# Kernel tuning notes

Measured on AMD Instinct MI355X. Metric: run time of the kernel, lower is better.

Reference implementation:

```python
import jax, jax.numpy as jnp
import numpy as np

K = 7          # local attention kernel size
PAD = 3        # (K-1)//2 so output spatial dims match input
GROUPS = 8

def unfold2d(x, k):
    # x: [B, C, H+k-1, W+k-1] -> patches [B, C, H, W, k*k] (kh-major, kw-minor, matching F.unfold)
    B, C, Hp, Wp = x.shape
    H, W = Hp - k + 1, Wp - k + 1
    return jnp.stack([x[:, :, i:i + H, j:j + W] for i in range(k) for j in range(k)], axis=-1)

def setup_inputs():
    key = jax.random.key(0)
    k1, k2, k3, k4, k5, k6 = jax.random.split(key, 6)
    B, Cin, H, W = 2, 256, 56, 56
    outc = 256
    scale = (2.0 / Cin) ** 0.5  # kaiming fan_out-ish init
    return {
        "feature_map": jax.random.normal(k1, (B, 2 * Cin, H, W), jnp.float32),
        "w_q": jax.random.normal(k2, (outc, Cin), jnp.float32) * scale,
        "w_k": jax.random.normal(k3, (outc, Cin), jnp.float32) * scale,
        "w_v": jax.random.normal(k4, (outc, Cin), jnp.float32) * scale,
        "rel_h": jax.random.normal(k5, (outc // 2, K), jnp.float32),
        "rel_w": jax.random.normal(k6, (outc // 2, K), jnp.float32),
    }

def reference(feature_map, w_q, w_k, w_v, rel_h, rel_w):
    B, C2, H, W = feature_map.shape
    Cin = C2 // 2
    fm_t0, fm_t1 = feature_map[:, :Cin], feature_map[:, Cin:]
    outc = w_q.shape[0]
    # 1x1 convs (bias=False)
    q = jnp.einsum('oc,bchw->bohw', w_q, fm_t1)                      # [B, outc, H, W]
    padded = jnp.pad(fm_t0, ((0, 0), (0, 0), (PAD, PAD), (PAD, PAD)))
    kk = jnp.einsum('oc,bchw->bohw', w_k, padded)
    vv = jnp.einsum('oc,bchw->bohw', w_v, padded)
    k_out = unfold2d(kk, K)                                          # [B, outc, H, W, K*K]
    v_out = unfold2d(vv, K)
    # relative position bias: first half channels get row bias, second half col bias
    half = outc // 2
    bias_h = jnp.broadcast_to(rel_h[:, :, None], (half, K, K)).reshape(half, K * K)
    bias_w = jnp.broadcast_to(rel_w[:, None, :], (half, K, K)).reshape(half, K * K)
    bias = jnp.concatenate([bias_h, bias_w], axis=0)                 # [outc, K*K]
    k_out = k_out + bias[None, :, None, None, :]
    G, Cg = GROUPS, outc // GROUPS
    qg = q.reshape(B, G, Cg, H, W)
    kg = k_out.reshape(B, G, Cg, H, W, K * K)
    vg = v_out.reshape(B, G, Cg, H, W, K * K)
    logits = jnp.einsum('bgchw,bgchwk->bghwk', qg, kg)
    wts = jax.nn.softmax(logits, axis=-1)
    out = jnp.einsum('bghwk,bgchwk->bgchw', wts, vg)
    return out.reshape(B, outc, H, W)
```

## Files before the change

kernel.cpp:

```cpp
#include <hip/hip_runtime.h>
#include <hip/hip_bf16.h>

#define B    2
#define CIN  256
#define H    56
#define W    56
#define OUTC 256
#define KS   7
#define PAD  3
#define G    8
#define CG   32
#define HP   62
#define WP   62
#define P1   (H * W)
#define P2   (HP * WP)

#define N1PAD 3200
#define N0PAD 3968

typedef __attribute__((ext_vector_type(2))) _Float16 h2;
typedef __attribute__((ext_vector_type(8))) _Float16 f16x8;
typedef __attribute__((ext_vector_type(8))) unsigned short ushort8;
typedef __attribute__((ext_vector_type(4))) float f32x4;

__device__ inline unsigned short f2h(float f) {
    const _Float16 h = (_Float16)f;
    return *(const unsigned short*)&h;
}

__device__ inline float fdot2(h2 a, h2 b, float c) {
#if defined(__has_builtin)
#if __has_builtin(__builtin_amdgcn_fdot2)
    return __builtin_amdgcn_fdot2(a, b, c, false);
#else
    return c + (float)a[0] * (float)b[0] + (float)a[1] * (float)b[1];
#endif
#else
    return c + (float)a[0] * (float)b[0] + (float)a[1] * (float)b[1];
#endif
}

__global__ __launch_bounds__(256) void prep_kernel(const float* __restrict__ fm,
                                                   const float* __restrict__ wq,
                                                   const float* __restrict__ wk,
                                                   const float* __restrict__ wv,
                                                   unsigned short* __restrict__ xt1,
                                                   unsigned short* __restrict__ xt0,
                                                   unsigned short* __restrict__ wqb,
                                                   unsigned short* __restrict__ wkvb) {
    const int u = blockIdx.x * 256 + threadIdx.x;
    if (u < 204800) {
        const int p  = u % 3200;
        const int t  = u / 3200;
        const int c8 = t & 31;
        const int b  = t >> 5;
        ushort8 o = {};
        if (p < P1) {
            const float* src = fm + ((size_t)(b * 512 + 256 + c8 * 8)) * P1 + p;
            #pragma unroll
            for (int j = 0; j < 8; ++j) o[j] = f2h(src[(size_t)j * P1]);
        }
        *(ushort8*)(xt1 + ((size_t)b * N1PAD + p) * CIN + c8 * 8) = o;
    } else if (u < 458752) {
        const int u2 = u - 204800;
        const int pp = u2 % 3968;
        const int t  = u2 / 3968;
        const int c8 = t & 31;
        const int b  = t >> 5;
        int srcoff = -1;
        if (pp < P2) {
            const int y = pp / WP, x = pp - y * WP;
            const int iy = y - PAD, ix = x - PAD;
            if (iy >= 0 && iy < H && ix >= 0 && ix < W) srcoff = iy * W + ix;
        }
        ushort8 o = {};
        if (srcoff >= 0) {
            const float* src = fm + ((size_t)(b * 512 + c8 * 8)) * P1 + srcoff;
            #pragma unroll
            for (int j = 0; j < 8; ++j) o[j] = f2h(src[(size_t)j * P1]);
        }
        *(ushort8*)(xt0 + ((size_t)b * N0PAD + pp) * CIN + c8 * 8) = o;
    } else {
        const int e = (u - 458752) * 8;
        const float* s;
        unsigned short* d;
        if (e < 65536)       { s = wq + e;            d = wqb + e; }
        else if (e < 131072) { s = wk + (e - 65536);  d = wkvb + (e - 65536); }
        else                 { s = wv + (e - 131072); d = wkvb + (e - 65536); }
        const float4 v0 = ((const float4*)s)[0];
        const float4 v1 = ((const float4*)s)[1];
        ushort8 o;
        o[0] = f2h(v0.x); o[1] = f2h(v0.y); o[2] = f2h(v0.z); o[3] = f2h(v0.w);
        o[4] = f2h(v1.x); o[5] = f2h(v1.y); o[6] = f2h(v1.z); o[7] = f2h(v1.w);
        *(ushort8*)d = o;
    }
}

#define ASTR 40
__global__ __launch_bounds__(256, 2) void gemm_kernel(const unsigned short* __restrict__ wqb,
                                                      const unsigned short* __restrict__ wkvb,
                                                      const unsigned short* __restrict__ xt1,
                                                      const unsigned short* __restrict__ xt0,
                                                      unsigned short* __restrict__ qi,
                                                      unsigned short* __restrict__ ki,
                                                      unsigned short* __restrict__ vi) {
    const int b = blockIdx.z;
    const bool isQ = blockIdx.y < 2;
    if (isQ && blockIdx.x >= 25) return;
    const int o0 = (isQ ? blockIdx.y : (blockIdx.y - 2)) * 128;
    const int n0 = blockIdx.x * 128;
    const unsigned short* Wb = isQ ? wqb : wkvb;
    const unsigned short* XtB = isQ ? (xt1 + (size_t)b * N1PAD * CIN)
                                    : (xt0 + (size_t)b * N0PAD * CIN);
    const int Nreal = isQ ? P1 : P2;
    const int Pstr  = isQ ? P1 : P2;

    __shared__ unsigned short Alds[128 * ASTR];
    __shared__ unsigned short Blds[128 * ASTR];
    const int tid = threadIdx.x;
    const int lane = tid & 63;
    const int wave = tid >> 6;
    const int wr = (wave >> 1) * 64;
    const int wc = (wave & 1) * 64;
    const int lrow = lane & 15;
    const int quad = lane >> 4;

    const unsigned short* Ag = Wb + (size_t)o0 * CIN;
    const unsigned short* Bg = XtB + (size_t)n0 * CIN;

    const int arow = tid >> 1;
    const int akc  = (tid & 1) * 16;
    const unsigned short* agp = Ag + (size_t)arow * CIN + akc;
    const unsigned short* bgp = Bg + (size_t)arow * CIN + akc;
    unsigned short* alp = Alds + arow * ASTR + akc;
    unsigned short* blp = Blds + arow * ASTR + akc;

    f32x4 acc[4][4] = {};

    f16x8 pa0 = *(const f16x8*)(agp);
    f16x8 pa1 = *(const f16x8*)(agp + 8);
    f16x8 pb0 = *(const f16x8*)(bgp);
    f16x8 pb1 = *(const f16x8*)(bgp + 8);

    for (int kb = 0; kb < CIN / 32; ++kb) {
        *(f16x8*)(alp)     = pa0;
        *(f16x8*)(alp + 8) = pa1;
        *(f16x8*)(blp)     = pb0;
        *(f16x8*)(blp + 8) = pb1;
        __syncthreads();
        if (kb < CIN / 32 - 1) {
            const int ko = (kb + 1) * 32;
            pa0 = *(const f16x8*)(agp + ko);
            pa1 = *(const f16x8*)(agp + ko + 8);
            pb0 = *(const f16x8*)(bgp + ko);
            pb1 = *(const f16x8*)(bgp + ko + 8);
        }
        f16x8 af[4], bfr[4];
        #pragma unroll
        for (int mi = 0; mi < 4; ++mi)
            af[mi] = *(const f16x8*)&Alds[(wr + mi * 16 + lrow) * ASTR + quad * 8];
        #pragma unroll
        for (int ni = 0; ni < 4; ++ni)
            bfr[ni] = *(const f16x8*)&Blds[(wc + ni * 16 + lrow) * ASTR + quad * 8];
        #pragma unroll
        for (int mi = 0; mi < 4; ++mi)
            #pragma unroll
            for (int ni = 0; ni < 4; ++ni)
                acc[mi][ni] = __builtin_amdgcn_mfma_f32_16x16x32_f16(af[mi], bfr[ni], acc[mi][ni], 0, 0, 0);
        __syncthreads();
    }

    #pragma unroll
    for (int mi = 0; mi < 4; ++mi) {
        const int gmBase = o0 + wr + mi * 16 + quad * 4;
        int ch0;
        unsigned short* base;
        if (isQ)              { ch0 = gmBase;       base = qi; }
        else if (gmBase < 256){ ch0 = gmBase;       base = ki; }
        else                  { ch0 = gmBase - 256; base = vi; }
        const int g   = ch0 >> 5;
        const int sub = (ch0 >> 3) & 3;
        const int l8  = ch0 & 7;
        unsigned short* pbase = base + ((((size_t)b * 8 + g) * 4 + sub) * Pstr) * 8 + l8;
        #pragma unroll
        for (int ni = 0; ni < 4; ++ni) {
            const int gn = n0 + wc + ni * 16 + lrow;
            if (gn < Nreal) {
                ushort4 pk;
                pk.x = f2h(acc[mi][ni][0]);
                pk.y = f2h(acc[mi][ni][1]);
                pk.z = f2h(acc[mi][ni][2]);
                pk.w = f2h(acc[mi][ni][3]);
                *(ushort4*)(pbase + (size_t)gn * 8) = pk;
            }
        }
    }
}

#define NPOS 496
__global__ __launch_bounds__(128) void attn_kernel(const unsigned short* __restrict__ qi,
                                                   const unsigned short* __restrict__ ki,
                                                   const unsigned short* __restrict__ vi,
                                                   const float* __restrict__ rel_h,
                                                   const float* __restrict__ rel_w,
                                                   float* __restrict__ out) {
    __shared__ f16x8 sbuf[2 * 992];

    const int b  = blockIdx.z;
    const int g  = blockIdx.y;
    const int r0 = blockIdx.x * 2;
    const int oc0 = g * CG;
    const int tid = threadIdx.x;
    const bool active = tid < 112;
    const int rr = tid / 56;
    const int cx = tid - rr * 56;
    const int pix = (r0 + rr) * W + cx;

    const size_t bg4 = ((size_t)b * 8 + g) * 4;
    const size_t rowoff8 = ((size_t)r0 * WP) * 8;

    f16x8* bufA = sbuf;
    f16x8* bufB = sbuf + 992;

    f16x8 qh[4];
    if (active) {
        #pragma unroll
        for (int sub = 0; sub < 4; ++sub)
            qh[sub] = *(const f16x8*)(qi + ((bg4 + sub) * P1 + pix) * 8);
    }

    f16x8 st[8];
    {
        const unsigned short* gb = ki + bg4 * P2 * 8 + rowoff8;
        #pragma unroll
        for (int it = 0; it < 8; ++it) {
            const int e = tid + it * 128;
            if (e < 992) {
                const int sl = (e >= 496);
                const int pos = e - (sl ? 496 : 0);
                st[it] = *(const f16x8*)(gb + ((size_t)sl * P2 + pos) * 8);
            }
        }
        #pragma unroll
        for (int it = 0; it < 8; ++it) {
            const int e = tid + it * 128;
            if (e < 992) bufA[e] = st[it];
        }
    }
    __syncthreads();

    {
        const unsigned short* gb = ki + (bg4 + 2) * P2 * 8 + rowoff8;
        #pragma unroll
        for (int it = 0; it < 8; ++it) {
            const int e = tid + it * 128;
            if (e < 992) {
                const int sl = (e >= 496);
                const int pos = e - (sl ? 496 : 0);
                st[it] = *(const f16x8*)(gb + ((size_t)sl * P2 + pos) * 8);
            }
        }
    }

    float logits[KS * KS];
    if (active) {
        const float* rel = (g < 4) ? (rel_h + oc0 * KS) : (rel_w + (oc0 - 128) * KS);
        float qf[32];
        #pragma unroll
        for (int sub = 0; sub < 4; ++sub)
            #pragma unroll
            for (int j = 0; j < 8; ++j)
                qf[sub * 8 + j] = (float)qh[sub][j];
        float biasdot[KS];
        #pragma unroll
        for (int t = 0; t < KS; ++t) {
            float s = 0.f;
            #pragma unroll
            for (int c = 0; c < 32; ++c) s += qf[c] * rel[c * KS + t];
            biasdot[t] = s;
        }
        #pragma unroll
        for (int i = 0; i < KS; ++i)
            #pragma unroll
            for (int j = 0; j < KS; ++j)
                logits[i * KS + j] = (g < 4) ? biasdot[i] : biasdot[j];

        #pragma unroll
        for (int sl = 0; sl < 2; ++sl) {
            const f16x8 qv = qh[sl];
            const h2 q0 = {qv[0], qv[1]}, q1 = {qv[2], qv[3]};
            const h2 q2 = {qv[4], qv[5]}, q3 = {qv[6], qv[7]};
            #pragma unroll
            for (int i = 0; i < KS; ++i) {
                const int eb = sl * NPOS + (rr + i) * WP + cx;
                #pragma unroll
                for (int j = 0; j < KS; ++j) {
                    const f16x8 kv = bufA[eb + j];
                    float s = logits[i * KS + j];
                    s = fdot2(q0, (h2){kv[0], kv[1]}, s);
                    s = fdot2(q1, (h2){kv[2], kv[3]}, s);
                    s = fdot2(q2, (h2){kv[4], kv[5]}, s);
                    s = fdot2(q3, (h2){kv[6], kv[7]}, s);
                    logits[i * KS + j] = s;
                }
            }
        }
    }
    #pragma unroll
    for (int it = 0; it < 8; ++it) {
        const int e = tid + it * 128;
        if (e < 992) bufB[e] = st[it];
    }
    __syncthreads();

    {
        const unsigned short* gb = vi + bg4 * P2 * 8 + rowoff8;
        #pragma unroll
        for (int it = 0; it < 8; ++it) {
            const int e = tid + it * 128;
            if (e < 992) {
                const int sl = (e >= 496);
                const int pos = e - (sl ? 496 : 0);
                st[it] = *(const f16x8*)(gb + ((size_t)sl * P2 + pos) * 8);
            }
        }
    }

    if (active) {
        #pragma unroll
        for (int sl = 0; sl < 2; ++sl) {
            const f16x8 qv = qh[2 + sl];
            const h2 q0 = {qv[0], qv[1]}, q1 = {qv[2], qv[3]};
            const h2 q2 = {qv[4], qv[5]}, q3 = {qv[6], qv[7]};
            #pragma unroll
            for (int i = 0; i < KS; ++i) {
                const int eb = sl * NPOS + (rr + i) * WP + cx;
                #pragma unroll
                for (int j = 0; j < KS; ++j) {
                    const f16x8 kv = bufB[eb + j];
                    float s = logits[i * KS + j];
                    s = fdot2(q0, (h2){kv[0], kv[1]}, s);
                    s = fdot2(q1, (h2){kv[2], kv[3]}, s);
                    s = fdot2(q2, (h2){kv[4], kv[5]}, s);
                    s = fdot2(q3, (h2){kv[6], kv[7]}, s);
                    logits[i * KS + j] = s;
                }
            }
        }
        float m = logits[0];
        #pragma unroll
        for (int t = 1; t < KS * KS; ++t) m = fmaxf(m, logits[t]);
        float sum = 0.f;
        #pragma unroll
        for (int t = 0; t < KS * KS; ++t) {
            const float e = __expf(logits[t] - m);
            logits[t] = e;
            sum += e;
        }
        const float inv = 1.f / sum;
        #pragma unroll
        for (int t = 0; t < KS * KS; ++t) logits[t] *= inv;
    }
    #pragma unroll
    for (int it = 0; it < 8; ++it) {
        const int e = tid + it * 128;
        if (e < 992) bufA[e] = st[it];
    }
    __syncthreads();

    {
        const unsigned short* gb = vi + (bg4 + 2) * P2 * 8 + rowoff8;
        #pragma unroll
        for (int it = 0; it < 8; ++it) {
            const int e = tid + it * 128;
            if (e < 992) {
                const int sl = (e >= 496);
                const int pos = e - (sl ? 496 : 0);
                st[it] = *(const f16x8*)(gb + ((size_t)sl * P2 + pos) * 8);
            }
        }
    }

    if (active) {
        #pragma unroll
        for (int sl = 0; sl < 2; ++sl) {
            float a[8] = {};
            #pragma unroll
            for (int i = 0; i < KS; ++i) {
                const int eb = sl * NPOS + (rr + i) * WP + cx;
                #pragma unroll
                for (int j = 0; j < KS; ++j) {
                    const f16x8 v = bufA[eb + j];
                    const float wt = logits[i * KS + j];
                    #pragma unroll
                    for (int c = 0; c < 8; ++c) a[c] += wt * (float)v[c];
                }
            }
            float* op = out + ((size_t)b * OUTC + oc0 + sl * 8) * P1 + pix;
            #pragma unroll
            for (int c = 0; c < 8; ++c) op[(size_t)c * P1] = a[c];
        }
    }
    #pragma unroll
    for (int it = 0; it < 8; ++it) {
        const int e = tid + it * 128;
        if (e < 992) bufB[e] = st[it];
    }
    __syncthreads();

    if (active) {
        #pragma unroll
        for (int sl = 0; sl < 2; ++sl) {
            float a[8] = {};
            #pragma unroll
            for (int i = 0; i < KS; ++i) {
                const int eb = sl * NPOS + (rr + i) * WP + cx;
                #pragma unroll
                for (int j = 0; j < KS; ++j) {
                    const f16x8 v = bufB[eb + j];
                    const float wt = logits[i * KS + j];
                    #pragma unroll
                    for (int c = 0; c < 8; ++c) a[c] += wt * (float)v[c];
                }
            }
            float* op = out + ((size_t)b * OUTC + oc0 + 16 + sl * 8) * P1 + pix;
            #pragma unroll
            for (int c = 0; c < 8; ++c) op[(size_t)c * P1] = a[c];
        }
    }
}

extern "C" void kernel_launch(void* const* d_in, const int* in_sizes, int n_in,
                              void* d_out, int out_size, void* d_ws, size_t ws_size,
                              hipStream_t stream) {
    const float* fm = (const float*)d_in[0];
    const float* wq = (const float*)d_in[1];
    const float* wk = (const float*)d_in[2];
    const float* wv = (const float*)d_in[3];
    const float* rh = (const float*)d_in[4];
    const float* rw = (const float*)d_in[5];
    float* out = (float*)d_out;

    unsigned short* ws = (unsigned short*)d_ws;
    unsigned short* xt1  = ws;
    unsigned short* xt0  = xt1 + (size_t)B * N1PAD * CIN;
    unsigned short* wqb  = xt0 + (size_t)B * N0PAD * CIN;
    unsigned short* wkvb = wqb + (size_t)OUTC * CIN;
    unsigned short* qi   = wkvb + (size_t)2 * OUTC * CIN;
    unsigned short* ki   = qi + (size_t)B * OUTC * P1;
    unsigned short* vi   = ki + (size_t)B * OUTC * P2;

    prep_kernel<<<1888, 256, 0, stream>>>(fm, wq, wk, wv, xt1, xt0, wqb, wkvb);
    gemm_kernel<<<dim3(31, 6, B), 256, 0, stream>>>(wqb, wkvb, xt1, xt0, qi, ki, vi);
    attn_kernel<<<dim3(H / 2, G, B), 128, 0, stream>>>(qi, ki, vi, rh, rw, out);
}
```

Measured before the change: 112.0 us.

## Fuse fp32-to-fp16 prep and padding into GEMM operand loads

Removes the separate prep kernel that transposed, padded and converted the feature map and weights to fp16. The GEMM now reads fp32 weights and the feature map directly, computes the padded source offset per column, and converts to fp16 while staging into LDS. This avoids one launch and a round trip of the transposed fp16 copies through global memory. In exchange, each GEMM block re-reads fp32 data (twice the bytes) with strided per-channel loads, and K/V blocks recompute the padding index math.

Result: faster. 109.2 us (-2.5%).

```diff
diff --git a/kernel.cpp b/kernel.cpp
--- a/kernel.cpp
+++ b/kernel.cpp
@@ -15,9 +15,6 @@
 #define P1   (H * W)
 #define P2   (HP * WP)
 
-#define N1PAD 3200
-#define N0PAD 3968
-
 typedef __attribute__((ext_vector_type(2))) _Float16 h2;
 typedef __attribute__((ext_vector_type(8))) _Float16 f16x8;
 typedef __attribute__((ext_vector_type(8))) unsigned short ushort8;
@@ -40,67 +37,11 @@
 #endif
 }
 
-__global__ __launch_bounds__(256) void prep_kernel(const float* __restrict__ fm,
-                                                   const float* __restrict__ wq,
-                                                   const float* __restrict__ wk,
-                                                   const float* __restrict__ wv,
-                                                   unsigned short* __restrict__ xt1,
-                                                   unsigned short* __restrict__ xt0,
-                                                   unsigned short* __restrict__ wqb,
-                                                   unsigned short* __restrict__ wkvb) {
-    const int u = blockIdx.x * 256 + threadIdx.x;
-    if (u < 204800) {
-        const int p  = u % 3200;
-        const int t  = u / 3200;
-        const int c8 = t & 31;
-        const int b  = t >> 5;
-        ushort8 o = {};
-        if (p < P1) {
-            const float* src = fm + ((size_t)(b * 512 + 256 + c8 * 8)) * P1 + p;
-            #pragma unroll
-            for (int j = 0; j < 8; ++j) o[j] = f2h(src[(size_t)j * P1]);
-        }
-        *(ushort8*)(xt1 + ((size_t)b * N1PAD + p) * CIN + c8 * 8) = o;
-    } else if (u < 458752) {
-        const int u2 = u - 204800;
-        const int pp = u2 % 3968;
-        const int t  = u2 / 3968;
-        const int c8 = t & 31;
-        const int b  = t >> 5;
-        int srcoff = -1;
-        if (pp < P2) {
-            const int y = pp / WP, x = pp - y * WP;
-            const int iy = y - PAD, ix = x - PAD;
-            if (iy >= 0 && iy < H && ix >= 0 && ix < W) srcoff = iy * W + ix;
-        }
-        ushort8 o = {};
-        if (srcoff >= 0) {
-            const float* src = fm + ((size_t)(b * 512 + c8 * 8)) * P1 + srcoff;
-            #pragma unroll
-            for (int j = 0; j < 8; ++j) o[j] = f2h(src[(size_t)j * P1]);
-        }
-        *(ushort8*)(xt0 + ((size_t)b * N0PAD + pp) * CIN + c8 * 8) = o;
-    } else {
-        const int e = (u - 458752) * 8;
-        const float* s;
-        unsigned short* d;
-        if (e < 65536)       { s = wq + e;            d = wqb + e; }
-        else if (e < 131072) { s = wk + (e - 65536);  d = wkvb + (e - 65536); }
-        else                 { s = wv + (e - 131072); d = wkvb + (e - 65536); }
-        const float4 v0 = ((const float4*)s)[0];
-        const float4 v1 = ((const float4*)s)[1];
-        ushort8 o;
-        o[0] = f2h(v0.x); o[1] = f2h(v0.y); o[2] = f2h(v0.z); o[3] = f2h(v0.w);
-        o[4] = f2h(v1.x); o[5] = f2h(v1.y); o[6] = f2h(v1.z); o[7] = f2h(v1.w);
-        *(ushort8*)d = o;
-    }
-}
-
 #define ASTR 40
-__global__ __launch_bounds__(256, 2) void gemm_kernel(const unsigned short* __restrict__ wqb,
-                                                      const unsigned short* __restrict__ wkvb,
-                                                      const unsigned short* __restrict__ xt1,
-                                                      const unsigned short* __restrict__ xt0,
+__global__ __launch_bounds__(256, 2) void gemm_kernel(const float* __restrict__ fm,
+                                                      const float* __restrict__ wq,
+                                                      const float* __restrict__ wk,
+                                                      const float* __restrict__ wv,
                                                       unsigned short* __restrict__ qi,
                                                       unsigned short* __restrict__ ki,
                                                       unsigned short* __restrict__ vi) {
@@ -109,11 +50,14 @@
     if (isQ && blockIdx.x >= 25) return;
     const int o0 = (isQ ? blockIdx.y : (blockIdx.y - 2)) * 128;
     const int n0 = blockIdx.x * 128;
-    const unsigned short* Wb = isQ ? wqb : wkvb;
-    const unsigned short* XtB = isQ ? (xt1 + (size_t)b * N1PAD * CIN)
-                                    : (xt0 + (size_t)b * N0PAD * CIN);
     const int Nreal = isQ ? P1 : P2;
     const int Pstr  = isQ ? P1 : P2;
+
+    const float* Wsrc;
+    int orow0;
+    if (isQ)            { Wsrc = wq; orow0 = o0; }
+    else if (o0 < 256)  { Wsrc = wk; orow0 = o0; }
+    else                { Wsrc = wv; orow0 = o0 - 256; }
 
     __shared__ unsigned short Alds[128 * ASTR];
     __shared__ unsigned short Blds[128 * ASTR];
@@ -125,35 +69,73 @@
     const int lrow = lane & 15;
     const int quad = lane >> 4;
 
-    const unsigned short* Ag = Wb + (size_t)o0 * CIN;
-    const unsigned short* Bg = XtB + (size_t)n0 * CIN;
-
-    const int arow = tid >> 1;
-    const int akc  = (tid & 1) * 16;
-    const unsigned short* agp = Ag + (size_t)arow * CIN + akc;
-    const unsigned short* bgp = Bg + (size_t)arow * CIN + akc;
+    const int arow = tid & 127;
+    const int akc  = (tid >> 7) * 16;
+
+    const int n = n0 + arow;
+    int srcoff = -1;
+    if (isQ) {
+        if (n < P1) srcoff = n;
+    } else {
+        if (n < P2) {
+            const int y = n / WP, x = n - y * WP;
+            const int iy = y - PAD, ix = x - PAD;
+            if (iy >= 0 && iy < H && ix >= 0 && ix < W) srcoff = iy * W + ix;
+        }
+    }
+    const float* fmB = fm + ((size_t)b * (2 * CIN) + (isQ ? CIN : 0)) * P1;
+    const float* wrow = Wsrc + (size_t)orow0 * CIN + (size_t)arow * CIN + akc;
+
     unsigned short* alp = Alds + arow * ASTR + akc;
     unsigned short* blp = Blds + arow * ASTR + akc;
 
     f32x4 acc[4][4] = {};
 
-    f16x8 pa0 = *(const f16x8*)(agp);
-    f16x8 pa1 = *(const f16x8*)(agp + 8);
-    f16x8 pb0 = *(const f16x8*)(bgp);
-    f16x8 pb1 = *(const f16x8*)(bgp + 8);
+    float av[16], bv[16];
+    {
+        const float4 a0 = ((const float4*)wrow)[0];
+        const float4 a1 = ((const float4*)wrow)[1];
+        const float4 a2 = ((const float4*)wrow)[2];
+        const float4 a3 = ((const float4*)wrow)[3];
+        av[0]=a0.x; av[1]=a0.y; av[2]=a0.z; av[3]=a0.w;
+        av[4]=a1.x; av[5]=a1.y; av[6]=a1.z; av[7]=a1.w;
+        av[8]=a2.x; av[9]=a2.y; av[10]=a2.z; av[11]=a2.w;
+        av[12]=a3.x; av[13]=a3.y; av[14]=a3.z; av[15]=a3.w;
+        #pragma unroll
+        for (int j = 0; j < 16; ++j)
+            bv[j] = (srcoff >= 0) ? fmB[(size_t)(akc + j) * P1 + srcoff] : 0.f;
+    }
 
     for (int kb = 0; kb < CIN / 32; ++kb) {
-        *(f16x8*)(alp)     = pa0;
-        *(f16x8*)(alp + 8) = pa1;
-        *(f16x8*)(blp)     = pb0;
-        *(f16x8*)(blp + 8) = pb1;
+        {
+            f16x8 p0, p1, p2, p3;
+            #pragma unroll
+            for (int j = 0; j < 8; ++j) {
+                p0[j] = (_Float16)av[j];
+                p1[j] = (_Float16)av[8 + j];
+                p2[j] = (_Float16)bv[j];
+                p3[j] = (_Float16)bv[8 + j];
+            }
+            *(f16x8*)(alp)     = p0;
+            *(f16x8*)(alp + 8) = p1;
+            *(f16x8*)(blp)     = p2;
+            *(f16x8*)(blp + 8) = p3;
+        }
         __syncthreads();
         if (kb < CIN / 32 - 1) {
-            const int ko = (kb + 1) * 32;
-            pa0 = *(const f16x8*)(agp + ko);
-            pa1 = *(const f16x8*)(agp + ko + 8);
-            pb0 = *(const f16x8*)(bgp + ko);
-            pb1 = *(const f16x8*)(bgp + ko + 8);
+            const int c0 = (kb + 1) * 32 + akc;
+            const float* wnext = wrow + (kb + 1) * 32;
+            const float4 a0 = ((const float4*)wnext)[0];
+            const float4 a1 = ((const float4*)wnext)[1];
+            const float4 a2 = ((const float4*)wnext)[2];
+            const float4 a3 = ((const float4*)wnext)[3];
+            av[0]=a0.x; av[1]=a0.y; av[2]=a0.z; av[3]=a0.w;
+            av[4]=a1.x; av[5]=a1.y; av[6]=a1.z; av[7]=a1.w;
+            av[8]=a2.x; av[9]=a2.y; av[10]=a2.z; av[11]=a2.w;
+            av[12]=a3.x; av[13]=a3.y; av[14]=a3.z; av[15]=a3.w;
+            #pragma unroll
+            for (int j = 0; j < 16; ++j)
+                bv[j] = (srcoff >= 0) ? fmB[(size_t)(c0 + j) * P1 + srcoff] : 0.f;
         }
         f16x8 af[4], bfr[4];
         #pragma unroll
@@ -175,9 +157,9 @@
         const int gmBase = o0 + wr + mi * 16 + quad * 4;
         int ch0;
         unsigned short* base;
-        if (isQ)              { ch0 = gmBase;       base = qi; }
-        else if (gmBase < 256){ ch0 = gmBase;       base = ki; }
-        else                  { ch0 = gmBase - 256; base = vi; }
+        if (isQ)               { ch0 = gmBase;       base = qi; }
+        else if (gmBase < 256) { ch0 = gmBase;       base = ki; }
+        else                   { ch0 = gmBase - 256; base = vi; }
         const int g   = ch0 >> 5;
         const int sub = (ch0 >> 3) & 3;
         const int l8  = ch0 & 7;
@@ -442,15 +424,10 @@
     float* out = (float*)d_out;
 
     unsigned short* ws = (unsigned short*)d_ws;
-    unsigned short* xt1  = ws;
-    unsigned short* xt0  = xt1 + (size_t)B * N1PAD * CIN;
-    unsigned short* wqb  = xt0 + (size_t)B * N0PAD * CIN;
-    unsigned short* wkvb = wqb + (size_t)OUTC * CIN;
-    unsigned short* qi   = wkvb + (size_t)2 * OUTC * CIN;
-    unsigned short* ki   = qi + (size_t)B * OUTC * P1;
-    unsigned short* vi   = ki + (size_t)B * OUTC * P2;
-
-    prep_kernel<<<1888, 256, 0, stream>>>(fm, wq, wk, wv, xt1, xt0, wqb, wkvb);
-    gemm_kernel<<<dim3(31, 6, B), 256, 0, stream>>>(wqb, wkvb, xt1, xt0, qi, ki, vi);
+    unsigned short* qi = ws;
+    unsigned short* ki = qi + (size_t)B * OUTC * P1;
+    unsigned short* vi = ki + (size_t)B * OUTC * P2;
+
+    gemm_kernel<<<dim3(31, 6, B), 256, 0, stream>>>(fm, wq, wk, wv, qi, ki, vi);
     attn_kernel<<<dim3(H / 2, G, B), 128, 0, stream>>>(qi, ki, vi, rh, rw, out);
 }
```
